# Optimization experiments

Hardware: AMD Instinct MI355X
Metric: run time of the kernel (lower is better)

## Reference

```python
import jax, jax.numpy as jnp
import numpy as np

GROUP_SIZE = 32
OUT_FEATURES = 4096
IN_FEATURES = 4096
NUM_GROUPS = OUT_FEATURES * IN_FEATURES // GROUP_SIZE  # 524288
PACKED_SIZE = (GROUP_SIZE + 1) // 2  # 16


def setup_inputs() -> dict:
    key = jax.random.key(0)
    k1, k2, k3, k4 = jax.random.split(key, 4)
    x = jax.random.normal(k1, (8, 2048, IN_FEATURES), dtype=jnp.float32)
    # two 3-bit values per byte -> valid packed values are in [0, 64)
    weight_packed = jax.random.randint(k2, (NUM_GROUPS, PACKED_SIZE), 0, 64, dtype=jnp.int32)
    weight_scales = jax.random.uniform(k3, (NUM_GROUPS,), minval=0.01, maxval=1.0).astype(jnp.float16)
    bias = jax.random.normal(k4, (OUT_FEATURES,)).astype(jnp.float16)
    return {"x": x, "weight_packed": weight_packed, "weight_scales": weight_scales, "bias": bias}


def _dequantize(weight_packed, weight_scales):
    # unpack: even positions = low 3 bits, odd positions = bits 3..5
    low = weight_packed & 7          # [G, P]
    high = (weight_packed >> 3) & 7  # [G, P]
    q = jnp.stack([low, high], axis=-1).reshape(NUM_GROUPS, GROUP_SIZE)  # interleaved [G, 32]
    # dequant: q/7 in [0,1] -> [-1,1] -> * per-group scale
    w = (q.astype(jnp.float32) * (2.0 / 7.0) - 1.0) * weight_scales.astype(jnp.float32)[:, None]
    return w.reshape(OUT_FEATURES, IN_FEATURES)


def reference(x, weight_packed, weight_scales, bias):
    W = _dequantize(weight_packed, weight_scales)  # [out, in] fp32
    # F.linear: x @ W.T + b
    return jnp.einsum('bsi,oi->bso', x, W) + bias.astype(jnp.float32)
```

## Files before the change

kernel.cpp:

```cpp
#include <hip/hip_runtime.h>


#define K_DIM 4096
#define N_DIM 4096
#define BM 128
#define BN 128
#define BK 64

typedef __bf16 bf16_t;
typedef __bf16 bf16x8 __attribute__((ext_vector_type(8)));
typedef float f32x4 __attribute__((ext_vector_type(4)));

__device__ __forceinline__ void gload16(const void* g, void* l) {
    __builtin_amdgcn_global_load_lds(
        (const __attribute__((address_space(1))) unsigned int*)g,
        (__attribute__((address_space(3))) unsigned int*)l, 16, 0, 0);
}

__global__ __launch_bounds__(256) void dequant_kernel(const int4* __restrict__ wp4,
                                                      const float* __restrict__ scales,
                                                      bf16x8* __restrict__ W) {
    const int t = blockIdx.x * 256 + threadIdx.x;
    const int4 p = wp4[t];
    const float s = scales[t >> 2];
    const float c = 2.0f / 7.0f;
    int v[4] = {p.x, p.y, p.z, p.w};
    bf16x8 o;
#pragma unroll
    for (int i = 0; i < 4; ++i) {
        float w0 = fmaf((float)(v[i] & 7), c, -1.0f) * s;
        float w1 = fmaf((float)((v[i] >> 3) & 7), c, -1.0f) * s;
        o[2 * i]     = (__bf16)w0;
        o[2 * i + 1] = (__bf16)w1;
    }
    W[t] = o;
}

__global__ __launch_bounds__(256) void convx_kernel(const float4* __restrict__ X4,
                                                    bf16x8* __restrict__ Xb) {
    const int t = blockIdx.x * 256 + threadIdx.x;
    float4 a = X4[2 * t];
    float4 b = X4[2 * t + 1];
    bf16x8 o;
    o[0] = (__bf16)a.x; o[1] = (__bf16)a.y; o[2] = (__bf16)a.z; o[3] = (__bf16)a.w;
    o[4] = (__bf16)b.x; o[5] = (__bf16)b.y; o[6] = (__bf16)b.z; o[7] = (__bf16)b.w;
    Xb[t] = o;
}

template <bool PRE>
__global__ __launch_bounds__(256) void gemm_kernel(const void* __restrict__ Ap,
                                                   const bf16_t* __restrict__ B,
                                                   const float* __restrict__ bias,
                                                   float* __restrict__ C) {
    __shared__ __align__(16) bf16_t As[BM * BK];
    __shared__ __align__(16) bf16_t Bs[BN * BK];

    const int tid  = threadIdx.x;
    const int lane = tid & 63;
    const int wv   = tid >> 6;
    const int wm   = (wv & 1) * 64;
    const int wn   = (wv >> 1) * 64;
    const int m0   = blockIdx.y * BM;
    const int n0   = blockIdx.x * BN;

    f32x4 acc[4][4];
#pragma unroll
    for (int i = 0; i < 4; ++i)
#pragma unroll
        for (int j = 0; j < 4; ++j) acc[i][j] = {0.f, 0.f, 0.f, 0.f};

    const int r8   = lane >> 3;
    const int kc   = (lane & 7) * 8;
    const int mrow = lane & 15;
    const int quad = lane >> 4;

    for (int k0 = 0; k0 < K_DIM; k0 += BK) {
        __syncthreads();
        if (PRE) {
            const bf16_t* A = (const bf16_t*)Ap;
#pragma unroll
            for (int c = 0; c < 4; ++c) {
                const int rowb = wv * 32 + c * 8;
                gload16(A + (size_t)(m0 + rowb + r8) * K_DIM + k0 + kc, &As[rowb * BK]);
                gload16(B + (size_t)(n0 + rowb + r8) * K_DIM + k0 + kc, &Bs[rowb * BK]);
            }
        } else {
            const float* A = (const float*)Ap;
            const int row = tid >> 1;
            const int kh  = (tid & 1) * 32;
            const float4* ga = (const float4*)(A + (size_t)(m0 + row) * K_DIM + k0 + kh);
            bf16x8* dst = (bf16x8*)&As[row * BK + kh];
#pragma unroll
            for (int c = 0; c < 4; ++c) {
                float4 u = ga[2 * c];
                float4 v = ga[2 * c + 1];
                bf16x8 o;
                o[0] = (__bf16)u.x; o[1] = (__bf16)u.y; o[2] = (__bf16)u.z; o[3] = (__bf16)u.w;
                o[4] = (__bf16)v.x; o[5] = (__bf16)v.y; o[6] = (__bf16)v.z; o[7] = (__bf16)v.w;
                dst[c] = o;
            }
#pragma unroll
            for (int c = 0; c < 4; ++c) {
                const int rowb = wv * 32 + c * 8;
                gload16(B + (size_t)(n0 + rowb + r8) * K_DIM + k0 + kc, &Bs[rowb * BK]);
            }
        }
        __syncthreads();

#pragma unroll
        for (int kk = 0; kk < BK; kk += 32) {
            bf16x8 af[4], bfr[4];
#pragma unroll
            for (int i = 0; i < 4; ++i)
                af[i] = *(const bf16x8*)&As[(wm + i * 16 + mrow) * BK + kk + quad * 8];
#pragma unroll
            for (int j = 0; j < 4; ++j)
                bfr[j] = *(const bf16x8*)&Bs[(wn + j * 16 + mrow) * BK + kk + quad * 8];
#pragma unroll
            for (int i = 0; i < 4; ++i)
#pragma unroll
                for (int j = 0; j < 4; ++j)
                    acc[i][j] = __builtin_amdgcn_mfma_f32_16x16x32_bf16(af[i], bfr[j],
                                                                        acc[i][j], 0, 0, 0);
        }
    }

    const int col   = lane & 15;
    const int rbase = (lane >> 4) * 4;
#pragma unroll
    for (int j = 0; j < 4; ++j) {
        const int n  = n0 + wn + j * 16 + col;
        const float bn = bias[n];
#pragma unroll
        for (int i = 0; i < 4; ++i) {
            const size_t base = (size_t)(m0 + wm + i * 16 + rbase) * N_DIM + n;
#pragma unroll
            for (int r = 0; r < 4; ++r)
                C[base + (size_t)r * N_DIM] = acc[i][j][r] + bn;
        }
    }
}

extern "C" void kernel_launch(void* const* d_in, const int* in_sizes, int n_in,
                              void* d_out, int out_size, void* d_ws, size_t ws_size,
                              hipStream_t stream) {
    const float* x      = (const float*)d_in[0];
    const int*   wp     = (const int*)d_in[1];
    const float* scales = (const float*)d_in[2];
    const float* bias   = (const float*)d_in[3];
    float*       out    = (float*)d_out;

    const int M = in_sizes[0] / K_DIM;

    bf16_t* Wb = (bf16_t*)d_ws;
    const size_t wbytes = (size_t)N_DIM * K_DIM * sizeof(bf16_t);
    bf16_t* Xb = (bf16_t*)((char*)d_ws + wbytes);
    const size_t need = wbytes + (size_t)M * K_DIM * sizeof(bf16_t);

    dequant_kernel<<<(N_DIM * K_DIM / 8) / 256, 256, 0, stream>>>(
        (const int4*)wp, scales, (bf16x8*)Wb);

    dim3 grid(N_DIM / BN, M / BM);
    if (ws_size >= need) {
        convx_kernel<<<((size_t)M * K_DIM / 8) / 256, 256, 0, stream>>>(
            (const float4*)x, (bf16x8*)Xb);
        gemm_kernel<true><<<grid, 256, 0, stream>>>(Xb, Wb, bias, out);
    } else {
        gemm_kernel<false><<<grid, 256, 0, stream>>>(x, Wb, bias, out);
    }
}
```

Measured before the change: 1.257 ms.

## Add 256x256 double-buffered GEMM with swizzled LDS and grouped tile order

```diff
diff --git a/kernel.cpp b/kernel.cpp
--- a/kernel.cpp
+++ b/kernel.cpp
@@ -3,9 +3,15 @@
 
 #define K_DIM 4096
 #define N_DIM 4096
+
 #define BM 128
 #define BN 128
 #define BK 64
+
+#define BM2 256
+#define BN2 256
+#define BK2 64
+#define NT2 (K_DIM / BK2)
 
 typedef __bf16 bf16_t;
 typedef __bf16 bf16x8 __attribute__((ext_vector_type(8)));
@@ -45,6 +51,120 @@
     o[0] = (__bf16)a.x; o[1] = (__bf16)a.y; o[2] = (__bf16)a.z; o[3] = (__bf16)a.w;
     o[4] = (__bf16)b.x; o[5] = (__bf16)b.y; o[6] = (__bf16)b.z; o[7] = (__bf16)b.w;
     Xb[t] = o;
+}
+
+__global__ __launch_bounds__(512, 2) void gemm256_kernel(const bf16_t* __restrict__ A,
+                                                         const bf16_t* __restrict__ B,
+                                                         const float* __restrict__ bias,
+                                                         float* __restrict__ C) {
+    __shared__ __align__(16) bf16_t As[2][BM2 * BK2];
+    __shared__ __align__(16) bf16_t Bs[2][BN2 * BK2];
+
+    const int tid  = threadIdx.x;
+    const int lane = tid & 63;
+    const int wv   = tid >> 6;
+    const int wm   = (wv >> 2) * 128;
+    const int wn   = (wv & 3) * 64;
+
+    const int nwg = gridDim.x;
+    const int bid = blockIdx.x;
+    const int swz = (bid & 7) * (nwg >> 3) + (bid >> 3);
+    const int n0  = (swz & 15) * BN2;
+    const int m0  = (swz >> 4) * BM2;
+
+    f32x4 acc[8][4];
+#pragma unroll
+    for (int i = 0; i < 8; ++i)
+#pragma unroll
+        for (int j = 0; j < 4; ++j) acc[i][j] = {0.f, 0.f, 0.f, 0.f};
+
+    const int r8  = lane >> 3;
+    const int csw = ((lane & 7) ^ r8) << 3;
+    const bf16_t* aSrc = A + (size_t)(m0 + wv * 8 + r8) * K_DIM + csw;
+    const bf16_t* bSrc = B + (size_t)(n0 + wv * 8 + r8) * K_DIM + csw;
+
+    auto stage = [&](int buf, int k0) {
+#pragma unroll
+        for (int r = 0; r < 4; ++r) {
+            gload16(aSrc + (size_t)(r * 64) * K_DIM + k0, &As[buf][(r * 64 + wv * 8) * BK2]);
+            gload16(bSrc + (size_t)(r * 64) * K_DIM + k0, &Bs[buf][(r * 64 + wv * 8) * BK2]);
+        }
+    };
+
+    const int mrow = lane & 15;
+    const int quad = lane >> 4;
+    const int m7   = mrow & 7;
+    const int sw0  = ((quad ^ m7) << 3);
+    const int sw1  = (((quad + 4) ^ m7) << 3);
+    const int offA0 = (wm + mrow) * BK2 + sw0;
+    const int offA1 = (wm + mrow) * BK2 + sw1;
+    const int offB0 = (wn + mrow) * BK2 + sw0;
+    const int offB1 = (wn + mrow) * BK2 + sw1;
+
+    stage(0, 0);
+    stage(1, BK2);
+
+    for (int t = 0; t < NT2; ++t) {
+        const int cur = t & 1;
+        if (t < NT2 - 1) {
+            asm volatile("s_waitcnt vmcnt(8)" ::: "memory");
+        } else {
+            asm volatile("s_waitcnt vmcnt(0)" ::: "memory");
+        }
+        __builtin_amdgcn_s_barrier();
+        asm volatile("" ::: "memory");
+
+        const bf16_t* as = &As[cur][0];
+        const bf16_t* bs = &Bs[cur][0];
+
+        bf16x8 a0[8], b0[4];
+#pragma unroll
+        for (int i = 0; i < 8; ++i) a0[i] = *(const bf16x8*)(as + offA0 + i * (16 * BK2));
+#pragma unroll
+        for (int j = 0; j < 4; ++j) b0[j] = *(const bf16x8*)(bs + offB0 + j * (16 * BK2));
+        __builtin_amdgcn_s_setprio(1);
+#pragma unroll
+        for (int i = 0; i < 8; ++i)
+#pragma unroll
+            for (int j = 0; j < 4; ++j)
+                acc[i][j] = __builtin_amdgcn_mfma_f32_16x16x32_bf16(a0[i], b0[j],
+                                                                    acc[i][j], 0, 0, 0);
+        __builtin_amdgcn_s_setprio(0);
+
+        bf16x8 a1[8], b1[4];
+#pragma unroll
+        for (int i = 0; i < 8; ++i) a1[i] = *(const bf16x8*)(as + offA1 + i * (16 * BK2));
+#pragma unroll
+        for (int j = 0; j < 4; ++j) b1[j] = *(const bf16x8*)(bs + offB1 + j * (16 * BK2));
+        __builtin_amdgcn_s_setprio(1);
+#pragma unroll
+        for (int i = 0; i < 8; ++i)
+#pragma unroll
+            for (int j = 0; j < 4; ++j)
+                acc[i][j] = __builtin_amdgcn_mfma_f32_16x16x32_bf16(a1[i], b1[j],
+                                                                    acc[i][j], 0, 0, 0);
+        __builtin_amdgcn_s_setprio(0);
+
+        asm volatile("" ::: "memory");
+        __builtin_amdgcn_s_barrier();
+        asm volatile("" ::: "memory");
+        if (t + 2 < NT2) stage(cur, (t + 2) * BK2);
+    }
+
+    const int col   = lane & 15;
+    const int rbase = (lane >> 4) * 4;
+#pragma unroll
+    for (int j = 0; j < 4; ++j) {
+        const int n  = n0 + wn + j * 16 + col;
+        const float bn = bias[n];
+#pragma unroll
+        for (int i = 0; i < 8; ++i) {
+            const size_t base = (size_t)(m0 + wm + i * 16 + rbase) * N_DIM + n;
+#pragma unroll
+            for (int r = 0; r < 4; ++r)
+                C[base + (size_t)r * N_DIM] = acc[i][j][r] + bn;
+        }
+    }
 }
 
 template <bool PRE>
@@ -160,12 +280,13 @@
     dequant_kernel<<<(N_DIM * K_DIM / 8) / 256, 256, 0, stream>>>(
         (const int4*)wp, scales, (bf16x8*)Wb);
 
-    dim3 grid(N_DIM / BN, M / BM);
-    if (ws_size >= need) {
+    if (ws_size >= need && (M % BM2) == 0) {
         convx_kernel<<<((size_t)M * K_DIM / 8) / 256, 256, 0, stream>>>(
             (const float4*)x, (bf16x8*)Xb);
-        gemm_kernel<true><<<grid, 256, 0, stream>>>(Xb, Wb, bias, out);
+        dim3 grid2((unsigned)((M / BM2) * (N_DIM / BN2)));
+        gemm256_kernel<<<grid2, 512, 0, stream>>>(Xb, Wb, bias, out);
     } else {
+        dim3 grid(N_DIM / BN, M / BM);
         gemm_kernel<false><<<grid, 256, 0, stream>>>(x, Wb, bias, out);
     }
 }
```

Result: faster. 1.070 ms (-14.9%).
